# Kernel tuning notes

Hardware: AMD Instinct MI355X
Metric: run time of the kernel (lower is better)

Reference implementation:

```python
import jax, jax.numpy as jnp
import numpy as np

K = 4          # conv kernel size
DIL = 3        # conv dilation
EPS = 1e-5     # rms eps inside gate kernel
NORM_EPS = 1e-5  # RMSNorm eps for value rms


def setup_inputs() -> dict:
    key = jax.random.key(0)
    ks = jax.random.split(key, 10)
    B, T, G, C, E = 2, 4096, 4, 1024, 1024
    return {
        "embeddings": jax.random.normal(ks[0], (B, T, E), jnp.float32),
        "hidden_states": jax.random.normal(ks[1], (B, T, G, C), jnp.float32),
        "key_w": jax.random.normal(ks[2], (G * C, E), jnp.float32) * 0.02,
        "key_b": jax.random.normal(ks[3], (G * C,), jnp.float32) * 0.02,
        "value_w": jax.random.normal(ks[4], (C, E), jnp.float32) * 0.02,
        "value_b": jax.random.normal(ks[5], (C,), jnp.float32) * 0.02,
        "w_key_norm": jax.random.uniform(ks[6], (G, C), jnp.float32, 0.5, 1.5),
        "w_query_norm": jax.random.uniform(ks[7], (G, C), jnp.float32, 0.5, 1.5),
        "w_norm": jax.random.uniform(ks[8], (G, C), jnp.float32, 0.5, 1.5),
        "conv_weight": jax.random.normal(ks[9], (G * C, K), jnp.float32) * 0.1,
    }


def reference(embeddings, hidden_states, key_w, key_b, value_w, value_b,
              w_key_norm, w_query_norm, w_norm, conv_weight):
    B, T, G, C = hidden_states.shape
    # projections
    k_all = (embeddings @ key_w.T + key_b).reshape(B, T, G, C)     # [B,T,G,C]
    q_all = hidden_states                                          # [B,T,G,C]
    vproj = embeddings @ value_w.T + value_b                       # [B,T,C]

    # gate kernel: per (b,t,g) RMS of key/query + weighted dot -> sign-sqrt-sigmoid gate
    rms_k = jnp.sqrt(jnp.mean(k_all * k_all, axis=-1) + EPS)       # [B,T,G]
    rms_q = jnp.sqrt(jnp.mean(q_all * q_all, axis=-1) + EPS)       # [B,T,G]
    dot = jnp.einsum('btgc,gc,btgc,gc->btg', k_all, w_key_norm, q_all, w_query_norm)
    gate_raw = dot / (rms_k * rms_q) / jnp.sqrt(jnp.float32(C))
    gate = jax.nn.sigmoid(jnp.where(gate_raw >= 0, 1.0, -1.0)
                          * jnp.sqrt(jnp.maximum(jnp.abs(gate_raw), 1e-6)))
    value = vproj[:, :, None, :] * gate[..., None]                 # [B,T,G,C]
    rms_v = jnp.sqrt(jnp.mean(value * value, axis=-1) + NORM_EPS)  # [B,T,G]

    # conv+residual kernel: per-group RMS-norm, dilated depthwise causal conv, SiLU, residual
    normed = value * (w_norm[None, None] / rms_v[..., None])       # [B,T,G,C]
    conv_w = conv_weight.reshape(G, C, K)                          # depthwise weights
    pad = (K - 1) * DIL
    xp = jnp.pad(normed, ((0, 0), (pad, 0), (0, 0), (0, 0)))
    # acc[b,t,g,c] = sum_k normed[b, t-(K-1-k)*DIL, g, c] * conv_w[g,c,k]
    acc = xp[:, 0:T] * conv_w[None, None, :, :, 0]
    for k in range(1, K):
        acc = acc + xp[:, k * DIL: k * DIL + T] * conv_w[None, None, :, :, k]
    acc = acc * jax.nn.sigmoid(acc)  # SiLU activation
    return value + acc
```

## Files before the change

### kernel.cpp

```cpp
#include <hip/hip_runtime.h>
#include <hip/hip_bf16.h>
#include <cstdint>
#include <cstddef>

using bf16 = __hip_bfloat16;

typedef __bf16 bf16x8_t __attribute__((ext_vector_type(8)));
typedef float  f32x4_t  __attribute__((ext_vector_type(4)));

static constexpr int Bb = 2;
static constexpr int Tt = 4096;
static constexpr int Gg = 4;
static constexpr int Cc = 1024;
static constexpr int Mm = Bb * Tt;
static constexpr int GC = Gg * Cc;

__device__ __forceinline__ float bfbits2f(unsigned u) {
  union { unsigned i; float f; } c; c.i = u << 16; return c.f;
}
__device__ __forceinline__ ushort f2bfbits(float v) {
  union { __hip_bfloat16 h; ushort u; } c; c.h = __float2bfloat16(v); return c.u;
}

__device__ __forceinline__ void store_val(bf16* p, float v)  { *p = __float2bfloat16(v); }
__device__ __forceinline__ void store_val(float* p, float v) { *p = v; }

__device__ __forceinline__ void gld_lds16(const ushort* g, ushort* l) {
  __builtin_amdgcn_global_load_lds(
      (const __attribute__((address_space(1))) void*)g,
      (__attribute__((address_space(3))) void*)l, 16, 0, 0);
}

__global__ __launch_bounds__(256)
void cvt_bf16(const float* __restrict__ in, ushort* __restrict__ out, int n4)
{
  const int i = blockIdx.x * 256 + threadIdx.x;
  if (i >= n4) return;
  const float4 v = ((const float4*)in)[i];
  ushort4 o;
  o.x = f2bfbits(v.x); o.y = f2bfbits(v.y);
  o.z = f2bfbits(v.z); o.w = f2bfbits(v.w);
  ((ushort4*)out)[i] = o;
}

__global__ __launch_bounds__(256)
void cvt_split(const float* __restrict__ in, ushort* __restrict__ hi,
               ushort* __restrict__ lo, int n4)
{
  const int i = blockIdx.x * 256 + threadIdx.x;
  if (i >= n4) return;
  const float4 v = ((const float4*)in)[i];
  ushort4 h, l;
  h.x = f2bfbits(v.x); l.x = f2bfbits(v.x - bfbits2f(h.x));
  h.y = f2bfbits(v.y); l.y = f2bfbits(v.y - bfbits2f(h.y));
  h.z = f2bfbits(v.z); l.z = f2bfbits(v.z - bfbits2f(h.z));
  h.w = f2bfbits(v.w); l.w = f2bfbits(v.w - bfbits2f(h.w));
  ((ushort4*)hi)[i] = h;
  ((ushort4*)lo)[i] = l;
}

__global__ __launch_bounds__(512, 2)
void gemm_key_fused(const ushort* __restrict__ embH, const ushort* __restrict__ embL,
                    const ushort* __restrict__ kwH,  const ushort* __restrict__ kwL,
                    const float* __restrict__ key_b, const float* __restrict__ hid,
                    const float* __restrict__ wkn,   const float* __restrict__ wqn,
                    float* __restrict__ k2_part, float* __restrict__ dot_part,
                    float* __restrict__ q2_part)
{
  constexpr int NT = 32;
  __shared__ __align__(16) ushort sA[2 * 16384];
  __shared__ __align__(16) ushort sB[2 * 16384];

  const int tid  = threadIdx.x;
  const int lane = tid & 63;
  const int wave = tid >> 6;
  const int wm   = wave & 1;
  const int wn   = wave >> 1;
  const int l15  = lane & 15;
  const int cH   = (lane >> 4) ^ (lane & 7);
  const int row0 = blockIdx.y * 256;
  const int col0 = blockIdx.x * 256;

  const int sRow = tid >> 3;
  const int schk = (tid & 7) ^ (sRow & 7);
  const ushort* aSel = (schk < 4) ? embH : embL;
  const ushort* bSel = (schk < 4) ? kwH  : kwL;
  const int sel8 = (schk & 3) * 8;
  const int wofs = wave * 512;

  auto stageA = [&](int rb, int u, int b) {
    const size_t co = (size_t)u * 32 + sel8;
    gld_lds16(aSel + (size_t)(row0 + rb + sRow) * Cc + co,
              sA + b * 16384 + (rb >> 6) * 4096 + wofs);
    gld_lds16(aSel + (size_t)(row0 + rb + 64 + sRow) * Cc + co,
              sA + b * 16384 + ((rb >> 6) + 1) * 4096 + wofs);
  };
  auto stageB = [&](int rb, int u, int b) {
    const size_t co = (size_t)u * 32 + sel8;
    gld_lds16(bSel + (size_t)(col0 + rb + sRow) * Cc + co,
              sB + b * 16384 + (rb >> 6) * 4096 + wofs);
    gld_lds16(bSel + (size_t)(col0 + rb + 64 + sRow) * Cc + co,
              sB + b * 16384 + ((rb >> 6) + 1) * 4096 + wofs);
  };

  f32x4_t acc[2][2][4][2] = {};

#define PHASE(QM, QN, STAGE, DOVM)                                          \
  {                                                                         \
    bf16x8_t afH[4], afL[4], bgH[2], bgL[2];                                \
    _Pragma("unroll") for (int mi = 0; mi < 4; ++mi) {                      \
      const int r = (QM) * 128 + wm * 64 + mi * 16 + l15;                   \
      const ushort* pa = bufA + r * 64;                                     \
      afH[mi] = *(const bf16x8_t*)(pa + cH * 8);                            \
      afL[mi] = *(const bf16x8_t*)(pa + (cH ^ 4) * 8);                      \
    }                                                                       \
    _Pragma("unroll") for (int ni = 0; ni < 2; ++ni) {                      \
      const int r = (QN) * 128 + wn * 32 + ni * 16 + l15;                   \
      const ushort* pb = bufB + r * 64;                                     \
      bgH[ni] = *(const bf16x8_t*)(pb + cH * 8);                            \
      bgL[ni] = *(const bf16x8_t*)(pb + (cH ^ 4) * 8);                      \
    }                                                                       \
    STAGE;                                                                  \
    asm volatile("s_barrier" ::: "memory");                                 \
    asm volatile("s_waitcnt lgkmcnt(0)" ::: "memory");                      \
    __builtin_amdgcn_s_setprio(1);                                          \
    _Pragma("unroll") for (int mi = 0; mi < 4; ++mi)                        \
      _Pragma("unroll") for (int ni = 0; ni < 2; ++ni) {                    \
        acc[QM][QN][mi][ni] = __builtin_amdgcn_mfma_f32_16x16x32_bf16(      \
            afH[mi], bgH[ni], acc[QM][QN][mi][ni], 0, 0, 0);                \
        acc[QM][QN][mi][ni] = __builtin_amdgcn_mfma_f32_16x16x32_bf16(      \
            afH[mi], bgL[ni], acc[QM][QN][mi][ni], 0, 0, 0);                \
        acc[QM][QN][mi][ni] = __builtin_amdgcn_mfma_f32_16x16x32_bf16(      \
            afL[mi], bgH[ni], acc[QM][QN][mi][ni], 0, 0, 0);                \
      }                                                                     \
    __builtin_amdgcn_s_setprio(0);                                          \
    if (DOVM) { asm volatile("s_waitcnt vmcnt(4)" ::: "memory"); }          \
    asm volatile("s_barrier" ::: "memory");                                 \
  }

  stageA(0, 0, 0); stageB(0, 0, 0); stageB(128, 0, 0); stageA(128, 0, 0);
  asm volatile("s_waitcnt vmcnt(4)" ::: "memory");
  asm volatile("s_barrier" ::: "memory");

  for (int u = 0; u < NT; ++u) {
    const int b = u & 1, nb = b ^ 1;
    const ushort* bufA = sA + b * 16384;
    const ushort* bufB = sB + b * 16384;
    const bool pf = (u + 1 < NT);
    PHASE(0, 0, if (pf) stageA(0, u + 1, nb),   1)
    PHASE(0, 1, if (pf) stageB(0, u + 1, nb),   1)
    PHASE(1, 0, if (pf) stageB(128, u + 1, nb), 0)
    PHASE(1, 1, if (pf) stageA(128, u + 1, nb), 1)
  }
#undef PHASE

  const int lrow = lane >> 4;
  const int lcol = lane & 15;
  const int g    = col0 >> 10;

#pragma unroll
  for (int qm = 0; qm < 2; ++qm) {
    float s2[4][4] = {}, su[4][4] = {}, sq[4][4] = {};
#pragma unroll
    for (int qn = 0; qn < 2; ++qn)
#pragma unroll
      for (int ni = 0; ni < 2; ++ni) {
        const int col = col0 + qn * 128 + wn * 32 + ni * 16 + lcol;
        const float kb = key_b[col];
        const float ww = wkn[col] * wqn[col];
#pragma unroll
        for (int mi = 0; mi < 4; ++mi) {
          const int rowb = row0 + qm * 128 + wm * 64 + mi * 16 + lrow * 4;
#pragma unroll
          for (int r = 0; r < 4; ++r) {
            const float q = hid[(size_t)(rowb + r) * GC + col];
            const float k = acc[qm][qn][mi][ni][r] + kb;
            s2[mi][r] += k * k;
            su[mi][r] += k * ww * q;
            sq[mi][r] += q * q;
          }
        }
      }
#pragma unroll
    for (int off = 1; off < 16; off <<= 1) {
#pragma unroll
      for (int mi = 0; mi < 4; ++mi)
#pragma unroll
        for (int r = 0; r < 4; ++r) {
          s2[mi][r] += __shfl_xor(s2[mi][r], off);
          su[mi][r] += __shfl_xor(su[mi][r], off);
          sq[mi][r] += __shfl_xor(sq[mi][r], off);
        }
    }
    if (lcol == 0) {
#pragma unroll
      for (int mi = 0; mi < 4; ++mi) {
        const int rowb = row0 + qm * 128 + wm * 64 + mi * 16 + lrow * 4;
#pragma unroll
        for (int r = 0; r < 4; ++r) {
          atomicAdd(&k2_part[(rowb + r) * Gg + g],  s2[mi][r]);
          atomicAdd(&dot_part[(rowb + r) * Gg + g], su[mi][r]);
          atomicAdd(&q2_part[(rowb + r) * Gg + g],  sq[mi][r]);
        }
      }
    }
  }
}

template <typename OutT>
__global__ __launch_bounds__(256, 4)
void gemm_bt(const ushort* __restrict__ A, const ushort* __restrict__ Bm,
             const float* __restrict__ bias, OutT* __restrict__ C,
             int M, int N, int K)
{
  __shared__ __align__(16) ushort sA[128 * 64];
  __shared__ __align__(16) ushort sB[128 * 64];

  const int tid  = threadIdx.x;
  const int lane = tid & 63;
  const int wave = tid >> 6;
  const int wm   = wave & 1;
  const int wn   = wave >> 1;
  const int row0 = blockIdx.y * 128;
  const int col0 = blockIdx.x * 128;

  const int srow = tid >> 3;
  const int scol = ((tid & 7) ^ (srow & 7)) * 8;
  ushort* aWB = sA + wave * 512;
  ushort* bWB = sB + wave * 512;

  f32x4_t acc[4][4] = {};

  for (int kt = 0; kt < K; kt += 64) {
#pragma unroll
    for (int p = 0; p < 4; ++p) {
      gld_lds16(A  + (size_t)(row0 + p * 32 + srow) * K + kt + scol,
                aWB + p * 2048);
      gld_lds16(Bm + (size_t)(col0 + p * 32 + srow) * K + kt + scol,
                bWB + p * 2048);
    }
    __syncthreads();

#pragma unroll
    for (int ks = 0; ks < 2; ++ks) {
      const int cb = ks * 4 + (lane >> 4);
      const int ce = ((cb ^ (lane & 7)) * 8);
      bf16x8_t af[4], bfr[4];
#pragma unroll
      for (int mi = 0; mi < 4; ++mi) {
        const int r = wm * 64 + mi * 16 + (lane & 15);
        af[mi] = *(const bf16x8_t*)(sA + r * 64 + ce);
      }
#pragma unroll
      for (int ni = 0; ni < 4; ++ni) {
        const int r = wn * 64 + ni * 16 + (lane & 15);
        bfr[ni] = *(const bf16x8_t*)(sB + r * 64 + ce);
      }
#pragma unroll
      for (int mi = 0; mi < 4; ++mi)
#pragma unroll
        for (int ni = 0; ni < 4; ++ni)
          acc[mi][ni] = __builtin_amdgcn_mfma_f32_16x16x32_bf16(
              af[mi], bfr[ni], acc[mi][ni], 0, 0, 0);
    }
    __syncthreads();
  }

  const int lrow = lane >> 4;
  const int lcol = lane & 15;
#pragma unroll
  for (int ni = 0; ni < 4; ++ni) {
    const int col = col0 + wn * 64 + ni * 16 + lcol;
    const float bv = bias[col];
#pragma unroll
    for (int mi = 0; mi < 4; ++mi) {
      const int rowb = row0 + wm * 64 + mi * 16 + lrow * 4;
#pragma unroll
      for (int r = 0; r < 4; ++r)
        store_val(&C[(size_t)(rowb + r) * N + col], acc[mi][ni][r] + bv);
    }
  }
}

__global__ __launch_bounds__(256)
void finalize_kernel(const float* __restrict__ vproj,
                     const float* __restrict__ k2_part,
                     const float* __restrict__ dot_part,
                     const float* __restrict__ q2_part,
                     float* __restrict__ gate_o, float* __restrict__ snorm_o)
{
  const int bt   = blockIdx.x;
  const int tid  = threadIdx.x;
  const int g    = tid >> 6;
  const int lane = tid & 63;

  const float4 v4 = ((const float4*)(vproj + (size_t)bt * Cc))[tid];
  float pv = v4.x * v4.x + v4.y * v4.y + v4.z * v4.z + v4.w * v4.w;
#pragma unroll
  for (int off = 32; off > 0; off >>= 1) pv += __shfl_xor(pv, off);
  __shared__ float wsum[4];
  if (lane == 0) wsum[g] = pv;
  __syncthreads();

  if (lane == 0) {
    const float mv = (wsum[0] + wsum[1] + wsum[2] + wsum[3]) * (1.0f / 1024.0f);
    const float sk = k2_part[bt * Gg + g];
    const float sd = dot_part[bt * Gg + g];
    const float sq = q2_part[bt * Gg + g];
    const float rk = sqrtf(sk * (1.0f / 1024.0f) + 1e-5f);
    const float rq = sqrtf(sq * (1.0f / 1024.0f) + 1e-5f);
    const float graw = sd / (rk * rq) * (1.0f / 32.0f);
    const float sgn = (graw >= 0.f) ? 1.f : -1.f;
    const float gate = 1.f / (1.f + expf(-sgn * sqrtf(fmaxf(fabsf(graw), 1e-6f))));
    const float rv = sqrtf(gate * gate * mv + 1e-5f);
    gate_o[bt * Gg + g]  = gate;
    snorm_o[bt * Gg + g] = gate / rv;
  }
}

static constexpr int CJ  = 128;
static constexpr int NCH = 11;

__global__ __launch_bounds__(256)
void conv_kernel(const float* __restrict__ vproj, const float* __restrict__ gate,
                 const float* __restrict__ snorm, const float* __restrict__ wnm,
                 const float* __restrict__ cw, float* __restrict__ out)
{
  int x = blockIdx.x;
  const int cb = x & 3;  x >>= 2;
  const int p  = x % 3;  x /= 3;
  const int ch = x % NCH; x /= NCH;
  const int g  = x & 3;  x >>= 2;
  const int b  = x;
  const int c  = cb * 256 + threadIdx.x;

  const float wn = wnm[g * Cc + c];
  const float4 w = ((const float4*)cw)[g * Cc + c];

  int t = p + 3 * (ch * CJ);
  if (t >= Tt) return;

  float n1 = 0.f, n2 = 0.f, n3 = 0.f;
#pragma unroll
  for (int h = 3; h >= 1; --h) {
    const int th = t - 3 * h;
    float nv = 0.f;
    if (th >= 0) {
      const int bt = b * Tt + th;
      nv = vproj[(size_t)bt * Cc + c] * snorm[bt * Gg + g] * wn;
    }
    n3 = n2; n2 = n1; n1 = nv;
  }

  for (int j = 0; j < CJ && t < Tt; ++j, t += 3) {
    const int bt = b * Tt + t;
    const float vp  = vproj[(size_t)bt * Cc + c];
    const float gt  = gate[bt * Gg + g];
    const float sn  = snorm[bt * Gg + g];
    const float cur = vp * sn * wn;
    const float a   = w.x * n3 + w.y * n2 + w.z * n1 + w.w * cur;
    const float si  = a / (1.f + __expf(-a));
    out[((size_t)bt * Gg + g) * Cc + c] = vp * gt + si;
    n3 = n2; n2 = n1; n1 = cur;
  }
}

extern "C" void kernel_launch(void* const* d_in, const int* in_sizes, int n_in,
                              void* d_out, int out_size, void* d_ws, size_t ws_size,
                              hipStream_t stream)
{
  const float* emb   = (const float*)d_in[0];
  const float* hid   = (const float*)d_in[1];
  const float* key_w = (const float*)d_in[2];
  const float* key_b = (const float*)d_in[3];
  const float* val_w = (const float*)d_in[4];
  const float* val_b = (const float*)d_in[5];
  const float* wkn   = (const float*)d_in[6];
  const float* wqn   = (const float*)d_in[7];
  const float* wnm   = (const float*)d_in[8];
  const float* cwt   = (const float*)d_in[9];
  float* out = (float*)d_out;

  char* ws = (char*)d_ws;
  ushort* embH  = (ushort*)ws;  ws += (size_t)Mm * Cc * 2;
  ushort* embL  = (ushort*)ws;  ws += (size_t)Mm * Cc * 2;
  ushort* kwH   = (ushort*)ws;  ws += (size_t)GC * Cc * 2;
  ushort* kwL   = (ushort*)ws;  ws += (size_t)GC * Cc * 2;
  ushort* vwB   = (ushort*)ws;  ws += (size_t)Cc * Cc * 2;
  float*  vproj = (float*)ws;   ws += (size_t)Mm * Cc * 4;
  float*  k2p   = (float*)ws;   ws += (size_t)Mm * Gg * 4;
  float*  dotp  = (float*)ws;   ws += (size_t)Mm * Gg * 4;
  float*  q2p   = (float*)ws;   ws += (size_t)Mm * Gg * 4;
  float*  gate  = (float*)ws;   ws += (size_t)Mm * Gg * 4;
  float*  snorm = (float*)ws;

  hipMemsetAsync(k2p, 0, (size_t)3 * Mm * Gg * 4, stream);

  dim3 blk(256);
  cvt_split<<<dim3((Mm * Cc / 4) / 256), blk, 0, stream>>>(emb,   embH, embL, Mm * Cc / 4);
  cvt_split<<<dim3((GC * Cc / 4) / 256), blk, 0, stream>>>(key_w, kwH,  kwL,  GC * Cc / 4);
  cvt_bf16 <<<dim3((Cc * Cc / 4) / 256), blk, 0, stream>>>(val_w, vwB,  Cc * Cc / 4);

  gemm_key_fused<<<dim3(GC / 256, Mm / 256), dim3(512), 0, stream>>>(
      embH, embL, kwH, kwL, key_b, hid, wkn, wqn, k2p, dotp, q2p);

  gemm_bt<float><<<dim3(Cc / 128, Mm / 128), blk, 0, stream>>>(
      embH, vwB, val_b, vproj, Mm, Cc, Cc);

  finalize_kernel<<<dim3(Mm), blk, 0, stream>>>(vproj, k2p, dotp, q2p, gate, snorm);

  const int nblocks = Bb * Gg * NCH * 3 * (Cc / 256);
  conv_kernel<<<dim3(nblocks), blk, 0, stream>>>(vproj, gate, snorm, wnm, cwt, out);
}
```

Baseline: 588.7 us.

## Restructure key GEMM main loop into single-barrier stage with fragment reuse

Replaces the four-phase ping-pong loop (two barriers per phase, interleaved partial prefetches) with one loop body per K step. All next-tile global-to-LDS loads are issued up front, B fragments and both A fragment halves are reused across the four quadrant MFMA groups, and a single vmcnt(0)/barrier closes each iteration. Launch bounds are relaxed to one block per SIMD group, giving more registers for the larger live fragment set. This cuts barrier and redundant LDS-read overhead, at the cost of fully draining global loads each iteration and possibly lower occupancy.

```diff
diff --git a/kernel.cpp b/kernel.cpp
--- a/kernel.cpp
+++ b/kernel.cpp
@@ -59,7 +59,7 @@
   ((ushort4*)lo)[i] = l;
 }
 
-__global__ __launch_bounds__(512, 2)
+__global__ __launch_bounds__(512, 1)
 void gemm_key_fused(const ushort* __restrict__ embH, const ushort* __restrict__ embL,
                     const ushort* __restrict__ kwH,  const ushort* __restrict__ kwL,
                     const float* __restrict__ key_b, const float* __restrict__ hid,
@@ -77,7 +77,7 @@
   const int wm   = wave & 1;
   const int wn   = wave >> 1;
   const int l15  = lane & 15;
-  const int cH   = (lane >> 4) ^ (lane & 7);
+  const int cHk  = (lane >> 4) ^ (lane & 7);
   const int row0 = blockIdx.y * 256;
   const int col0 = blockIdx.x * 256;
 
@@ -105,54 +105,68 @@
 
   f32x4_t acc[2][2][4][2] = {};
 
-#define PHASE(QM, QN, STAGE, DOVM)                                          \
-  {                                                                         \
-    bf16x8_t afH[4], afL[4], bgH[2], bgL[2];                                \
-    _Pragma("unroll") for (int mi = 0; mi < 4; ++mi) {                      \
-      const int r = (QM) * 128 + wm * 64 + mi * 16 + l15;                   \
-      const ushort* pa = bufA + r * 64;                                     \
-      afH[mi] = *(const bf16x8_t*)(pa + cH * 8);                            \
-      afL[mi] = *(const bf16x8_t*)(pa + (cH ^ 4) * 8);                      \
-    }                                                                       \
+#define MFMA3(QM, QN, AH, AL, BH, BL)                                       \
+  _Pragma("unroll") for (int mi = 0; mi < 4; ++mi)                          \
     _Pragma("unroll") for (int ni = 0; ni < 2; ++ni) {                      \
-      const int r = (QN) * 128 + wn * 32 + ni * 16 + l15;                   \
-      const ushort* pb = bufB + r * 64;                                     \
-      bgH[ni] = *(const bf16x8_t*)(pb + cH * 8);                            \
-      bgL[ni] = *(const bf16x8_t*)(pb + (cH ^ 4) * 8);                      \
-    }                                                                       \
-    STAGE;                                                                  \
-    asm volatile("s_barrier" ::: "memory");                                 \
-    asm volatile("s_waitcnt lgkmcnt(0)" ::: "memory");                      \
-    __builtin_amdgcn_s_setprio(1);                                          \
-    _Pragma("unroll") for (int mi = 0; mi < 4; ++mi)                        \
-      _Pragma("unroll") for (int ni = 0; ni < 2; ++ni) {                    \
-        acc[QM][QN][mi][ni] = __builtin_amdgcn_mfma_f32_16x16x32_bf16(      \
-            afH[mi], bgH[ni], acc[QM][QN][mi][ni], 0, 0, 0);                \
-        acc[QM][QN][mi][ni] = __builtin_amdgcn_mfma_f32_16x16x32_bf16(      \
-            afH[mi], bgL[ni], acc[QM][QN][mi][ni], 0, 0, 0);                \
-        acc[QM][QN][mi][ni] = __builtin_amdgcn_mfma_f32_16x16x32_bf16(      \
-            afL[mi], bgH[ni], acc[QM][QN][mi][ni], 0, 0, 0);                \
-      }                                                                     \
-    __builtin_amdgcn_s_setprio(0);                                          \
-    if (DOVM) { asm volatile("s_waitcnt vmcnt(4)" ::: "memory"); }          \
-    asm volatile("s_barrier" ::: "memory");                                 \
-  }
+      acc[QM][QN][mi][ni] = __builtin_amdgcn_mfma_f32_16x16x32_bf16(        \
+          AH[mi], BH[ni], acc[QM][QN][mi][ni], 0, 0, 0);                    \
+      acc[QM][QN][mi][ni] = __builtin_amdgcn_mfma_f32_16x16x32_bf16(        \
+          AH[mi], BL[ni], acc[QM][QN][mi][ni], 0, 0, 0);                    \
+      acc[QM][QN][mi][ni] = __builtin_amdgcn_mfma_f32_16x16x32_bf16(        \
+          AL[mi], BH[ni], acc[QM][QN][mi][ni], 0, 0, 0);                    \
+    }
 
   stageA(0, 0, 0); stageB(0, 0, 0); stageB(128, 0, 0); stageA(128, 0, 0);
-  asm volatile("s_waitcnt vmcnt(4)" ::: "memory");
-  asm volatile("s_barrier" ::: "memory");
+  asm volatile("s_waitcnt vmcnt(0)" ::: "memory");
+  __builtin_amdgcn_s_barrier();
 
   for (int u = 0; u < NT; ++u) {
     const int b = u & 1, nb = b ^ 1;
     const ushort* bufA = sA + b * 16384;
     const ushort* bufB = sB + b * 16384;
-    const bool pf = (u + 1 < NT);
-    PHASE(0, 0, if (pf) stageA(0, u + 1, nb),   1)
-    PHASE(0, 1, if (pf) stageB(0, u + 1, nb),   1)
-    PHASE(1, 0, if (pf) stageB(128, u + 1, nb), 0)
-    PHASE(1, 1, if (pf) stageA(128, u + 1, nb), 1)
-  }
-#undef PHASE
+    if (u + 1 < NT) {
+      stageA(0, u + 1, nb);   stageB(0, u + 1, nb);
+      stageB(128, u + 1, nb); stageA(128, u + 1, nb);
+    }
+
+    bf16x8_t b0H[2], b0L[2], b1H[2], b1L[2];
+#pragma unroll
+    for (int ni = 0; ni < 2; ++ni) {
+      const ushort* p0 = bufB + (wn * 32 + ni * 16 + l15) * 64;
+      const ushort* p1 = bufB + (128 + wn * 32 + ni * 16 + l15) * 64;
+      b0H[ni] = *(const bf16x8_t*)(p0 + cHk * 8);
+      b0L[ni] = *(const bf16x8_t*)(p0 + (cHk ^ 4) * 8);
+      b1H[ni] = *(const bf16x8_t*)(p1 + cHk * 8);
+      b1L[ni] = *(const bf16x8_t*)(p1 + (cHk ^ 4) * 8);
+    }
+    bf16x8_t a0H[4], a0L[4];
+#pragma unroll
+    for (int mi = 0; mi < 4; ++mi) {
+      const ushort* pa = bufA + (wm * 64 + mi * 16 + l15) * 64;
+      a0H[mi] = *(const bf16x8_t*)(pa + cHk * 8);
+      a0L[mi] = *(const bf16x8_t*)(pa + (cHk ^ 4) * 8);
+    }
+    __builtin_amdgcn_s_setprio(1);
+    MFMA3(0, 0, a0H, a0L, b0H, b0L)
+    __builtin_amdgcn_s_setprio(0);
+    bf16x8_t a1H[4], a1L[4];
+#pragma unroll
+    for (int mi = 0; mi < 4; ++mi) {
+      const ushort* pa = bufA + (128 + wm * 64 + mi * 16 + l15) * 64;
+      a1H[mi] = *(const bf16x8_t*)(pa + cHk * 8);
+      a1L[mi] = *(const bf16x8_t*)(pa + (cHk ^ 4) * 8);
+    }
+    __builtin_amdgcn_s_setprio(1);
+    MFMA3(0, 1, a0H, a0L, b1H, b1L)
+    MFMA3(1, 0, a1H, a1L, b0H, b0L)
+    MFMA3(1, 1, a1H, a1L, b1H, b1L)
+    __builtin_amdgcn_s_setprio(0);
+
+    asm volatile("s_waitcnt lgkmcnt(0)" ::: "memory");
+    asm volatile("s_waitcnt vmcnt(0)" ::: "memory");
+    __builtin_amdgcn_s_barrier();
+  }
+#undef MFMA3
 
   const int lrow = lane >> 4;
   const int lcol = lane & 15;
```

Result: no change. 584.9 us (-0.6%).
